# Optimization experiments

Measured on AMD Instinct MI355X. Metric: run time of the kernel, lower is better.

## Reference

```python
import jax, jax.numpy as jnp
import numpy as np

B, NV, NE = 32, 8192, 65536
SUBSTEPS = 8
DT = 0.01
K_SPRING = 1.0e4   # spring stiffness
CG_ITERS = 20      # fixed CG iterations for the implicit solve
EPS = 1e-12


def setup_inputs() -> dict:
    key = jax.random.key(0)
    k0, k1, k2, k3, k4, k5 = jax.random.split(key, 6)
    # small actuation signals per spring (rest-length modulation)
    input_action = jax.random.normal(k0, (B, NE), dtype=jnp.float32) * 0.05
    # random spring graph with guaranteed i != j
    edge_i = jax.random.randint(k1, (NE,), 0, NV, dtype=jnp.int32)
    off = jax.random.randint(k2, (NE,), 1, NV, dtype=jnp.int32)
    edge_j = ((edge_i + off) % NV).astype(jnp.int32)
    pos0 = jax.random.normal(k3, (B, NV, 3), dtype=jnp.float32) * 0.5
    vel0 = jnp.zeros((B, NV, 3), dtype=jnp.float32)
    # rest lengths near the initial configuration so the system starts close to equilibrium
    d0 = pos0[0, edge_i] - pos0[0, edge_j]
    rest_len = jnp.linalg.norm(d0, axis=-1) + 1e-2
    mass = jax.random.uniform(k4, (NV,), dtype=jnp.float32) + 0.5
    return {"input_action": input_action, "pos0": pos0, "vel0": vel0,
            "rest_len": rest_len, "mass": mass,
            "edge_i": edge_i, "edge_j": edge_j}


def _bdot(a, b):
    # per-batch inner product, keepdims for broadcasting: [B,1,1]
    return jnp.sum(a * b, axis=(1, 2), keepdims=True)


def _spring_force(pos, rest_eff, ei, ej):
    # pos: [B,NV,3], rest_eff: [B,NE]
    d = pos[:, ei] - pos[:, ej]                       # [B,NE,3]
    l = jnp.linalg.norm(d, axis=-1, keepdims=True)    # [B,NE,1]
    dirn = d / jnp.maximum(l, 1e-6)
    fe = -K_SPRING * (l - rest_eff[..., None]) * dirn # [B,NE,3]
    f = jnp.zeros_like(pos).at[:, ei].add(fe).at[:, ej].add(-fe)
    return f


def _matvec(x, mass, ei, ej):
    # A x = M x + dt^2 * k * L x  (graph Laplacian Hessian approximation)
    d = x[:, ei] - x[:, ej]
    Lx = jnp.zeros_like(x).at[:, ei].add(d).at[:, ej].add(-d)
    return mass[None, :, None] * x + (DT * DT * K_SPRING) * Lx


def _cg_solve(b, mass, ei, ej):
    x = jnp.zeros_like(b)
    r = b
    p = r
    rs = _bdot(r, r)

    def body(carry, _):
        x, r, p, rs = carry
        Ap = _matvec(p, mass, ei, ej)
        alpha = rs / (_bdot(p, Ap) + EPS)
        x = x + alpha * p
        r = r - alpha * Ap
        rs_new = _bdot(r, r)
        p = r + (rs_new / (rs + EPS)) * p
        return (x, r, p, rs_new), None

    (x, _, _, _), _ = jax.lax.scan(body, (x, r, p, rs), None, length=CG_ITERS)
    return x


def reference(input_action, pos0, vel0, rest_len, mass, edge_i, edge_j):
    gravity = jnp.array([0.0, -9.8, 0.0], dtype=pos0.dtype)
    rest_eff = rest_len[None, :] * (1.0 + input_action)  # actuated rest lengths [B,NE]
    m3 = mass[None, :, None]

    def step(carry, _):
        pos, vel = carry
        f = _spring_force(pos, rest_eff, edge_i, edge_j) + m3 * gravity
        b = m3 * vel + DT * f                  # implicit Euler RHS
        v_new = _cg_solve(b, mass, edge_i, edge_j)
        pos_new = pos + DT * v_new
        return (pos_new, v_new), pos_new

    _, traj = jax.lax.scan(step, (pos0, vel0), None, length=SUBSTEPS)
    # traj: [SUBSTEPS, B, NV, 3] -> [B, SUBSTEPS, NV, 3]
    return jnp.transpose(traj, (1, 0, 2, 3))
```

## Files before the change

kernel.cpp:

```cpp
#include <hip/hip_runtime.h>
#include <hip/hip_cooperative_groups.h>
#include <math.h>

namespace cg = cooperative_groups;

#define NVERT 8192
#define NEDGE 65536
#define NSUB 8
#define NCG 20
#define GRID 256
#define BLOCK 1024
#define DT 0.01f
#define KS 10000.0f
#define NGRP 16
#define GSIZE 16

struct Params {
  const float* action;
  const float* pos0;
  const float* vel0;
  const float* rest_len;
  const float* mass;
  const int* edge_i;
  const int* edge_j;
  float* out;
  float2* posXY;
  float*  posZ;
  float2 *QXY0, *QXY1;
  float  *QZ0,  *QZ1;
  float* rest_eff;
  int* adj_off;
  int* adjE_off;
  int* row_ptr;
  int* cursor;
  double* Pd;
  double* Gd;
  unsigned* bar;
};

union U64F2 { unsigned long long u; float2 f; };
union U32F  { unsigned u; float f; };
union U64D  { unsigned long long u; double d; };

__device__ __forceinline__ float2 ld2_dev(const float2* p) {
  U64F2 r;
  r.u = __hip_atomic_load((const unsigned long long*)p, __ATOMIC_RELAXED, __HIP_MEMORY_SCOPE_AGENT);
  return r.f;
}
__device__ __forceinline__ void st2_dev(float2* p, float2 v) {
  U64F2 r; r.f = v;
  __hip_atomic_store((unsigned long long*)p, r.u, __ATOMIC_RELAXED, __HIP_MEMORY_SCOPE_AGENT);
}
__device__ __forceinline__ float ldf_dev(const float* p) {
  U32F r;
  r.u = __hip_atomic_load((const unsigned*)p, __ATOMIC_RELAXED, __HIP_MEMORY_SCOPE_AGENT);
  return r.f;
}
__device__ __forceinline__ void stf_dev(float* p, float v) {
  U32F r; r.f = v;
  __hip_atomic_store((unsigned*)p, r.u, __ATOMIC_RELAXED, __HIP_MEMORY_SCOPE_AGENT);
}
__device__ __forceinline__ double lddbl_dev(const double* p) {
  U64D r;
  r.u = __hip_atomic_load((const unsigned long long*)p, __ATOMIC_RELAXED, __HIP_MEMORY_SCOPE_AGENT);
  return r.d;
}
__device__ __forceinline__ void stdbl_dev(double* p, double v) {
  U64D r; r.d = v;
  __hip_atomic_store((unsigned long long*)p, r.u, __ATOMIC_RELAXED, __HIP_MEMORY_SCOPE_AGENT);
}

__device__ __forceinline__ void fast_bar(unsigned* bar, unsigned ep) {
  __syncthreads();
  if (threadIdx.x == 0) {
    const unsigned g = blockIdx.x >> 4;
    __hip_atomic_fetch_add(bar + g * 32, 1u,
                           __ATOMIC_RELAXED, __HIP_MEMORY_SCOPE_AGENT);
    const unsigned tgt = GSIZE * ep;
    for (;;) {
      bool ok = true;
#pragma unroll
      for (int i = 0; i < NGRP; ++i)
        ok &= (__hip_atomic_load(bar + i * 32,
                                 __ATOMIC_RELAXED, __HIP_MEMORY_SCOPE_AGENT) >= tgt);
      if (ok) break;
      __builtin_amdgcn_s_sleep(1);
    }
  }
  __syncthreads();
}

__device__ __forceinline__ void fast_bar_red(unsigned* bar, unsigned ep,
                                             const double* Pd, double* Gd, int par,
                                             int* lflag) {
  __syncthreads();
  const unsigned g = blockIdx.x >> 4;
  if (threadIdx.x == 0) {
    const unsigned old = __hip_atomic_fetch_add(bar + g * 32, 1u,
                          __ATOMIC_RELAXED, __HIP_MEMORY_SCOPE_AGENT);
    *lflag = (old == GSIZE * ep - 1);
  }
  __syncthreads();
  if (*lflag) {
    if (threadIdx.x < 96) {
      const double* base = Pd + (size_t)par * 256 * 96 + (size_t)(g * GSIZE) * 96
                           + threadIdx.x;
      double s = 0.0;
#pragma unroll
      for (int j = 0; j < GSIZE; ++j) s += lddbl_dev(base + j * 96);
      stdbl_dev(&Gd[(size_t)par * NGRP * 96 + g * 96 + threadIdx.x], s);
    }
    __syncthreads();
    if (threadIdx.x == 0)
      __hip_atomic_store(bar + (NGRP + 1 + g) * 32, ep,
                         __ATOMIC_RELAXED, __HIP_MEMORY_SCOPE_AGENT);
  }
  if (threadIdx.x == 0) {
    for (;;) {
      bool ok = true;
#pragma unroll
      for (int i = 0; i < NGRP; ++i)
        ok &= (__hip_atomic_load(bar + (NGRP + 1 + i) * 32,
                                 __ATOMIC_RELAXED, __HIP_MEMORY_SCOPE_AGENT) >= ep);
      if (ok) break;
      __builtin_amdgcn_s_sleep(1);
    }
  }
  __syncthreads();
}

__device__ __forceinline__ void publish_store(double* Pd, int par, double d0, double d1,
                                              double d2, double* lds) {
  d0 += __shfl_down(d0, 32);
  d1 += __shfl_down(d1, 32);
  d2 += __shfl_down(d2, 32);
  const int lane = threadIdx.x & 63, w = threadIdx.x >> 6;
  if (lane < 32) {
    lds[w * 96 + lane] = d0;
    lds[w * 96 + 32 + lane] = d1;
    lds[w * 96 + 64 + lane] = d2;
  }
  __syncthreads();
  if (threadIdx.x < 96) {
    double s = 0.0;
#pragma unroll
    for (int ww = 0; ww < BLOCK / 64; ++ww) s += lds[ww * 96 + threadIdx.x];
    stdbl_dev(&Pd[(size_t)par * 256 * 96 + (size_t)blockIdx.x * 96 + threadIdx.x], s);
  }
}

__device__ __forceinline__ void reduce_small(const double* Gd, int par,
                                             double* lds_part, double* lds_acc) {
  const int tid = threadIdx.x;
  const double* base = Gd + (size_t)par * NGRP * 96;
  lds_part[tid] = lddbl_dev(base + tid);
  if (tid < NGRP * 96 - BLOCK)
    lds_part[BLOCK + tid] = lddbl_dev(base + BLOCK + tid);
  __syncthreads();
  if (tid < 96) {
    double s = 0.0;
#pragma unroll
    for (int g = 0; g < NGRP; ++g) s += lds_part[g * 96 + tid];
    lds_acc[tid] = s;
  }
  __syncthreads();
}

__global__ void __launch_bounds__(BLOCK) mass_spring_kernel(Params P) {
  cg::grid_group grid = cg::this_grid();
  __shared__ double lds_red[(BLOCK / 64) * 96];
  __shared__ double lds_part[NGRP * 96];
  __shared__ double lds_acc[96];
  __shared__ int lds_scan[BLOCK];
  __shared__ int lds_flag;

  const int tid = threadIdx.x;
  const int gtid = blockIdx.x * BLOCK + tid;
  const int b = tid & 31;
  const int v = gtid >> 5;
  const int vb = v * 32 + b;
  const int b8 = b * 8, b4 = b * 4;
  unsigned ep = 0;

  for (int i = gtid; i < NEDGE * 32; i += GRID * BLOCK) {
    const int e = i >> 5, bb = i & 31;
    P.rest_eff[e * 32 + bb] = P.rest_len[e] * (1.0f + P.action[bb * NEDGE + e]);
  }
  float3 pv, vv;
  pv.x = P.pos0[(b * NVERT + v) * 3 + 0];
  pv.y = P.pos0[(b * NVERT + v) * 3 + 1];
  pv.z = P.pos0[(b * NVERT + v) * 3 + 2];
  vv.x = P.vel0[(b * NVERT + v) * 3 + 0];
  vv.y = P.vel0[(b * NVERT + v) * 3 + 1];
  vv.z = P.vel0[(b * NVERT + v) * 3 + 2];
  st2_dev(&P.posXY[vb], make_float2(pv.x, pv.y));
  stf_dev(&P.posZ[vb], pv.z);
  if (gtid < NVERT) P.cursor[gtid] = 0;
  if (gtid < (2 * NGRP + 1) * 32) P.bar[gtid] = 0u;
  grid.sync();

  if (gtid < NEDGE) {
    atomicAdd(&P.cursor[P.edge_i[gtid]], 1);
    atomicAdd(&P.cursor[P.edge_j[gtid]], 1);
  }
  grid.sync();

  if (blockIdx.x == 0) {
    const int base = tid * (NVERT / BLOCK);
    int loc[NVERT / BLOCK];
    int sum = 0;
#pragma unroll
    for (int i = 0; i < NVERT / BLOCK; ++i) { loc[i] = P.cursor[base + i]; sum += loc[i]; }
    lds_scan[tid] = sum;
    __syncthreads();
    for (int off = 1; off < BLOCK; off <<= 1) {
      int t = 0;
      if (tid >= off) t = lds_scan[tid - off];
      __syncthreads();
      if (tid >= off) lds_scan[tid] += t;
      __syncthreads();
    }
    int run = lds_scan[tid] - sum;
#pragma unroll
    for (int i = 0; i < NVERT / BLOCK; ++i) {
      P.row_ptr[base + i] = run;
      P.cursor[base + i] = run;
      run += loc[i];
    }
    if (tid == BLOCK - 1) P.row_ptr[NVERT] = run;
  }
  grid.sync();

  if (gtid < NEDGE) {
    const int ei = P.edge_i[gtid], ej = P.edge_j[gtid];
    const int ai = atomicAdd(&P.cursor[ei], 1);
    P.adj_off[ai] = ej * 256; P.adjE_off[ai] = gtid * 128;
    const int aj = atomicAdd(&P.cursor[ej], 1);
    P.adj_off[aj] = ei * 256; P.adjE_off[aj] = gtid * 128;
  }
  grid.sync();

  const float m_v = P.mass[v];
  const int rbeg = P.row_ptr[v], rend = P.row_ptr[v + 1];
  const float degf = (float)(rend - rbeg);

  float2* qXYrd = P.QXY0; float2* qXYwr = P.QXY1;
  float*  qZrd  = P.QZ0;  float*  qZwr  = P.QZ1;
  int pub = 0;

  for (int s = 0; s < NSUB; ++s) {
    float fx = 0.f, fy = 0.f, fz = 0.f;
#pragma unroll 4
    for (int a = rbeg; a < rend; ++a) {
      const int off = P.adj_off[a];
      const float2 pxy = ld2_dev((const float2*)((const char*)P.posXY + off + b8));
      const float  puz = ldf_dev((const float*)((const char*)P.posZ + (off >> 1) + b4));
      const float re = *(const float*)((const char*)P.rest_eff + P.adjE_off[a] + b4);
      const float dx = pv.x - pxy.x, dy = pv.y - pxy.y, dz = pv.z - puz;
      const float l = sqrtf(dx * dx + dy * dy + dz * dz);
      const float coef = -KS * (l - re) / fmaxf(l, 1e-6f);
      fx += coef * dx; fy += coef * dy; fz += coef * dz;
    }
    float3 rv;
    rv.x = m_v * vv.x + DT * fx;
    rv.y = m_v * vv.y + DT * (fy - 9.8f * m_v);
    rv.z = m_v * vv.z + DT * fz;
    st2_dev(&qXYrd[vb], make_float2(rv.x, rv.y));
    stf_dev(&qZrd[vb], rv.z);
    float3 xacc = make_float3(0.f, 0.f, 0.f);
    float3 pc = rv;
    float3 ap;
    float3 Sr, Sp;
    fast_bar(P.bar, ++ep);

    for (int k = 0; k < NCG; ++k) {
      if (k == 0) {
        float sx = 0.f, sy = 0.f, sz = 0.f;
#pragma unroll 4
        for (int a = rbeg; a < rend; ++a) {
          const int off = P.adj_off[a];
          const float2 qxy = ld2_dev((const float2*)((const char*)qXYrd + off + b8));
          const float  qz  = ldf_dev((const float*)((const char*)qZrd + (off >> 1) + b4));
          sx += qxy.x; sy += qxy.y; sz += qz;
        }
        Sr = make_float3(sx, sy, sz);
        Sp = Sr;
        ap.x = (m_v + degf) * pc.x - Sp.x;
        ap.y = (m_v + degf) * pc.y - Sp.y;
        ap.z = (m_v + degf) * pc.z - Sp.z;
      } else {
        const double* gbase = P.Gd + (size_t)((pub + 1) & 1) * NGRP * 96;
        const double gval0 = lddbl_dev(gbase + tid);
        double gval1 = 0.0;
        if (tid < NGRP * 96 - BLOCK) gval1 = lddbl_dev(gbase + BLOCK + tid);
        float sx = 0.f, sy = 0.f, sz = 0.f;
#pragma unroll 4
        for (int a = rbeg; a < rend; ++a) {
          const int off = P.adj_off[a];
          const float2 qxy = ld2_dev((const float2*)((const char*)qXYrd + off + b8));
          const float  qz  = ldf_dev((const float*)((const char*)qZrd + (off >> 1) + b4));
          sx += qxy.x; sy += qxy.y; sz += qz;
        }
        lds_part[tid] = gval0;
        if (tid < NGRP * 96 - BLOCK) lds_part[BLOCK + tid] = gval1;
        __syncthreads();
        if (tid < 96) {
          double s = 0.0;
#pragma unroll
          for (int g = 0; g < NGRP; ++g) s += lds_part[g * 96 + tid];
          lds_acc[tid] = s;
        }
        __syncthreads();
        const double rsx = lds_acc[b];
        const double pq  = lds_acc[32 + b];
        const double qq  = lds_acc[64 + b];
        const float alpha = (float)(rsx / (pq + 1e-12));
        const double rs_rec = (double)alpha * (double)alpha * qq - rsx;
        const float beta = (float)(rs_rec / (rsx + 1e-12));
        xacc.x += alpha * pc.x; xacc.y += alpha * pc.y; xacc.z += alpha * pc.z;
        rv.x -= alpha * ap.x; rv.y -= alpha * ap.y; rv.z -= alpha * ap.z;
        Sr.x -= alpha * sx; Sr.y -= alpha * sy; Sr.z -= alpha * sz;
        pc.x = rv.x + beta * pc.x; pc.y = rv.y + beta * pc.y; pc.z = rv.z + beta * pc.z;
        Sp.x = Sr.x + beta * Sp.x; Sp.y = Sr.y + beta * Sp.y; Sp.z = Sr.z + beta * Sp.z;
        ap.x = (m_v + degf) * pc.x - Sp.x;
        ap.y = (m_v + degf) * pc.y - Sp.y;
        ap.z = (m_v + degf) * pc.z - Sp.z;
      }
      if (k != NCG - 1) {
        st2_dev(&qXYwr[vb], make_float2(ap.x, ap.y));
        stf_dev(&qZwr[vb], ap.z);
      }
      publish_store(P.Pd, pub & 1,
                    (double)(rv.x * rv.x) + (double)(rv.y * rv.y) + (double)(rv.z * rv.z),
                    (double)(pc.x * ap.x) + (double)(pc.y * ap.y) + (double)(pc.z * ap.z),
                    (double)(ap.x * ap.x) + (double)(ap.y * ap.y) + (double)(ap.z * ap.z),
                    lds_red);
      fast_bar_red(P.bar, ++ep, P.Pd, P.Gd, pub & 1, &lds_flag);
      ++pub;
      float2* t2 = qXYrd; qXYrd = qXYwr; qXYwr = t2;
      float*  t1 = qZrd;  qZrd  = qZwr;  qZwr  = t1;
    }

    {
      reduce_small(P.Gd, (pub + 1) & 1, lds_part, lds_acc);
      const double rsx = lds_acc[b];
      const double pq  = lds_acc[32 + b];
      const float alpha = (float)(rsx / (pq + 1e-12));
      xacc.x += alpha * pc.x; xacc.y += alpha * pc.y; xacc.z += alpha * pc.z;
      vv = xacc;
      pv.x += DT * vv.x; pv.y += DT * vv.y; pv.z += DT * vv.z;
      st2_dev(&P.posXY[vb], make_float2(pv.x, pv.y));
      stf_dev(&P.posZ[vb], pv.z);
      float* o = P.out + ((size_t)(b * NSUB + s) * NVERT + (size_t)v) * 3;
      o[0] = pv.x; o[1] = pv.y; o[2] = pv.z;
      fast_bar(P.bar, ++ep);
    }
  }
}

extern "C" void kernel_launch(void* const* d_in, const int* in_sizes, int n_in,
                              void* d_out, int out_size, void* d_ws, size_t ws_size,
                              hipStream_t stream) {
  Params P;
  P.action = (const float*)d_in[0];
  P.pos0 = (const float*)d_in[1];
  P.vel0 = (const float*)d_in[2];
  P.rest_len = (const float*)d_in[3];
  P.mass = (const float*)d_in[4];
  P.edge_i = (const int*)d_in[5];
  P.edge_j = (const int*)d_in[6];
  P.out = (float*)d_out;

  char* w = (char*)d_ws;
  auto alloc = [&](size_t bytes) {
    char* p = w;
    w += (bytes + 255) & ~(size_t)255;
    return p;
  };
  const size_t xy_bytes = (size_t)NVERT * 32 * sizeof(float2);
  const size_t z_bytes  = (size_t)NVERT * 32 * sizeof(float);
  P.posXY = (float2*)alloc(xy_bytes);
  P.posZ  = (float*)alloc(z_bytes);
  P.QXY0  = (float2*)alloc(xy_bytes);
  P.QXY1  = (float2*)alloc(xy_bytes);
  P.QZ0   = (float*)alloc(z_bytes);
  P.QZ1   = (float*)alloc(z_bytes);
  P.rest_eff = (float*)alloc((size_t)NEDGE * 32 * sizeof(float));
  P.adj_off  = (int*)alloc((size_t)2 * NEDGE * sizeof(int));
  P.adjE_off = (int*)alloc((size_t)2 * NEDGE * sizeof(int));
  P.row_ptr  = (int*)alloc((size_t)(NVERT + 1) * sizeof(int));
  P.cursor   = (int*)alloc((size_t)NVERT * sizeof(int));
  P.Pd       = (double*)alloc((size_t)2 * 256 * 96 * sizeof(double));
  P.Gd       = (double*)alloc((size_t)2 * NGRP * 96 * sizeof(double));
  P.bar      = (unsigned*)alloc((size_t)(2 * NGRP + 1) * 32 * sizeof(unsigned));

  void* args[] = { &P };
  hipLaunchCooperativeKernel(reinterpret_cast<void*>(mass_spring_kernel),
                             dim3(GRID), dim3(BLOCK), args, 0, stream);
}
```

Before: 2.089 ms.

## Replace two-level grid reduction with cumulative f64 atomics across striped rows

Each block now adds its per-batch CG dot-product partials with float64 atomics into one of four striped accumulator rows, instead of writing partials that group leaders combine hierarchically. The accumulators are never reset. Each block recovers the per-iteration value by subtracting the previous running total. This drops the second barrier phase and the group-level reduction pass, leaving a single plain grid barrier per CG iteration. In exchange it adds atomic contention on 384 doubles. Differencing running sums could also lose precision as the totals grow, and atomic ordering makes the reductions non-deterministic.

```diff
diff --git a/kernel.cpp b/kernel.cpp
--- a/kernel.cpp
+++ b/kernel.cpp
@@ -14,6 +14,7 @@
 #define KS 10000.0f
 #define NGRP 16
 #define GSIZE 16
+#define NROW 4
 
 struct Params {
   const float* action;
@@ -33,8 +34,7 @@
   int* adjE_off;
   int* row_ptr;
   int* cursor;
-  double* Pd;
-  double* Gd;
+  double* A;
   unsigned* bar;
 };
 
@@ -65,9 +65,9 @@
   r.u = __hip_atomic_load((const unsigned long long*)p, __ATOMIC_RELAXED, __HIP_MEMORY_SCOPE_AGENT);
   return r.d;
 }
-__device__ __forceinline__ void stdbl_dev(double* p, double v) {
-  U64D r; r.d = v;
-  __hip_atomic_store((unsigned long long*)p, r.u, __ATOMIC_RELAXED, __HIP_MEMORY_SCOPE_AGENT);
+
+__device__ __forceinline__ void atomic_add_f64_dev(double* p, double v) {
+  unsafeAtomicAdd(p, v);
 }
 
 __device__ __forceinline__ void fast_bar(unsigned* bar, unsigned ep) {
@@ -90,47 +90,8 @@
   __syncthreads();
 }
 
-__device__ __forceinline__ void fast_bar_red(unsigned* bar, unsigned ep,
-                                             const double* Pd, double* Gd, int par,
-                                             int* lflag) {
-  __syncthreads();
-  const unsigned g = blockIdx.x >> 4;
-  if (threadIdx.x == 0) {
-    const unsigned old = __hip_atomic_fetch_add(bar + g * 32, 1u,
-                          __ATOMIC_RELAXED, __HIP_MEMORY_SCOPE_AGENT);
-    *lflag = (old == GSIZE * ep - 1);
-  }
-  __syncthreads();
-  if (*lflag) {
-    if (threadIdx.x < 96) {
-      const double* base = Pd + (size_t)par * 256 * 96 + (size_t)(g * GSIZE) * 96
-                           + threadIdx.x;
-      double s = 0.0;
-#pragma unroll
-      for (int j = 0; j < GSIZE; ++j) s += lddbl_dev(base + j * 96);
-      stdbl_dev(&Gd[(size_t)par * NGRP * 96 + g * 96 + threadIdx.x], s);
-    }
-    __syncthreads();
-    if (threadIdx.x == 0)
-      __hip_atomic_store(bar + (NGRP + 1 + g) * 32, ep,
-                         __ATOMIC_RELAXED, __HIP_MEMORY_SCOPE_AGENT);
-  }
-  if (threadIdx.x == 0) {
-    for (;;) {
-      bool ok = true;
-#pragma unroll
-      for (int i = 0; i < NGRP; ++i)
-        ok &= (__hip_atomic_load(bar + (NGRP + 1 + i) * 32,
-                                 __ATOMIC_RELAXED, __HIP_MEMORY_SCOPE_AGENT) >= ep);
-      if (ok) break;
-      __builtin_amdgcn_s_sleep(1);
-    }
-  }
-  __syncthreads();
-}
-
-__device__ __forceinline__ void publish_store(double* Pd, int par, double d0, double d1,
-                                              double d2, double* lds) {
+__device__ __forceinline__ void publish_atomic(double* Arow, double d0, double d1,
+                                               double d2, double* lds) {
   d0 += __shfl_down(d0, 32);
   d1 += __shfl_down(d1, 32);
   d2 += __shfl_down(d2, 32);
@@ -145,34 +106,15 @@
     double s = 0.0;
 #pragma unroll
     for (int ww = 0; ww < BLOCK / 64; ++ww) s += lds[ww * 96 + threadIdx.x];
-    stdbl_dev(&Pd[(size_t)par * 256 * 96 + (size_t)blockIdx.x * 96 + threadIdx.x], s);
-  }
-}
-
-__device__ __forceinline__ void reduce_small(const double* Gd, int par,
-                                             double* lds_part, double* lds_acc) {
-  const int tid = threadIdx.x;
-  const double* base = Gd + (size_t)par * NGRP * 96;
-  lds_part[tid] = lddbl_dev(base + tid);
-  if (tid < NGRP * 96 - BLOCK)
-    lds_part[BLOCK + tid] = lddbl_dev(base + BLOCK + tid);
-  __syncthreads();
-  if (tid < 96) {
-    double s = 0.0;
-#pragma unroll
-    for (int g = 0; g < NGRP; ++g) s += lds_part[g * 96 + tid];
-    lds_acc[tid] = s;
-  }
-  __syncthreads();
+    atomic_add_f64_dev(Arow + threadIdx.x, s);
+  }
 }
 
 __global__ void __launch_bounds__(BLOCK) mass_spring_kernel(Params P) {
   cg::grid_group grid = cg::this_grid();
   __shared__ double lds_red[(BLOCK / 64) * 96];
-  __shared__ double lds_part[NGRP * 96];
   __shared__ double lds_acc[96];
   __shared__ int lds_scan[BLOCK];
-  __shared__ int lds_flag;
 
   const int tid = threadIdx.x;
   const int gtid = blockIdx.x * BLOCK + tid;
@@ -181,6 +123,8 @@
   const int vb = v * 32 + b;
   const int b8 = b * 8, b4 = b * 4;
   unsigned ep = 0;
+  double prevq = 0.0;
+  double* const Arow = P.A + (size_t)(blockIdx.x & (NROW - 1)) * 96;
 
   for (int i = gtid; i < NEDGE * 32; i += GRID * BLOCK) {
     const int e = i >> 5, bb = i & 31;
@@ -197,6 +141,7 @@
   stf_dev(&P.posZ[vb], pv.z);
   if (gtid < NVERT) P.cursor[gtid] = 0;
   if (gtid < (2 * NGRP + 1) * 32) P.bar[gtid] = 0u;
+  if (gtid < NROW * 96) P.A[gtid] = 0.0;
   grid.sync();
 
   if (gtid < NEDGE) {
@@ -246,7 +191,6 @@
 
   float2* qXYrd = P.QXY0; float2* qXYwr = P.QXY1;
   float*  qZrd  = P.QZ0;  float*  qZwr  = P.QZ1;
-  int pub = 0;
 
   for (int s = 0; s < NSUB; ++s) {
     float fx = 0.f, fy = 0.f, fz = 0.f;
@@ -289,10 +233,13 @@
         ap.y = (m_v + degf) * pc.y - Sp.y;
         ap.z = (m_v + degf) * pc.z - Sp.z;
       } else {
-        const double* gbase = P.Gd + (size_t)((pub + 1) & 1) * NGRP * 96;
-        const double gval0 = lddbl_dev(gbase + tid);
-        double gval1 = 0.0;
-        if (tid < NGRP * 96 - BLOCK) gval1 = lddbl_dev(gbase + BLOCK + tid);
+        double av0, av1, av2, av3;
+        if (tid < 96) {
+          av0 = lddbl_dev(P.A + tid);
+          av1 = lddbl_dev(P.A + 96 + tid);
+          av2 = lddbl_dev(P.A + 192 + tid);
+          av3 = lddbl_dev(P.A + 288 + tid);
+        }
         float sx = 0.f, sy = 0.f, sz = 0.f;
 #pragma unroll 4
         for (int a = rbeg; a < rend; ++a) {
@@ -301,14 +248,10 @@
           const float  qz  = ldf_dev((const float*)((const char*)qZrd + (off >> 1) + b4));
           sx += qxy.x; sy += qxy.y; sz += qz;
         }
-        lds_part[tid] = gval0;
-        if (tid < NGRP * 96 - BLOCK) lds_part[BLOCK + tid] = gval1;
-        __syncthreads();
         if (tid < 96) {
-          double s = 0.0;
-#pragma unroll
-          for (int g = 0; g < NGRP; ++g) s += lds_part[g * 96 + tid];
-          lds_acc[tid] = s;
+          const double anow = (av0 + av1) + (av2 + av3);
+          lds_acc[tid] = anow - prevq;
+          prevq = anow;
         }
         __syncthreads();
         const double rsx = lds_acc[b];
@@ -330,19 +273,24 @@
         st2_dev(&qXYwr[vb], make_float2(ap.x, ap.y));
         stf_dev(&qZwr[vb], ap.z);
       }
-      publish_store(P.Pd, pub & 1,
-                    (double)(rv.x * rv.x) + (double)(rv.y * rv.y) + (double)(rv.z * rv.z),
-                    (double)(pc.x * ap.x) + (double)(pc.y * ap.y) + (double)(pc.z * ap.z),
-                    (double)(ap.x * ap.x) + (double)(ap.y * ap.y) + (double)(ap.z * ap.z),
-                    lds_red);
-      fast_bar_red(P.bar, ++ep, P.Pd, P.Gd, pub & 1, &lds_flag);
-      ++pub;
+      publish_atomic(Arow,
+                     (double)(rv.x * rv.x) + (double)(rv.y * rv.y) + (double)(rv.z * rv.z),
+                     (double)(pc.x * ap.x) + (double)(pc.y * ap.y) + (double)(pc.z * ap.z),
+                     (double)(ap.x * ap.x) + (double)(ap.y * ap.y) + (double)(ap.z * ap.z),
+                     lds_red);
+      fast_bar(P.bar, ++ep);
       float2* t2 = qXYrd; qXYrd = qXYwr; qXYwr = t2;
       float*  t1 = qZrd;  qZrd  = qZwr;  qZwr  = t1;
     }
 
     {
-      reduce_small(P.Gd, (pub + 1) & 1, lds_part, lds_acc);
+      if (tid < 96) {
+        const double anow = (lddbl_dev(P.A + tid) + lddbl_dev(P.A + 96 + tid))
+                          + (lddbl_dev(P.A + 192 + tid) + lddbl_dev(P.A + 288 + tid));
+        lds_acc[tid] = anow - prevq;
+        prevq = anow;
+      }
+      __syncthreads();
       const double rsx = lds_acc[b];
       const double pq  = lds_acc[32 + b];
       const float alpha = (float)(rsx / (pq + 1e-12));
@@ -390,8 +338,7 @@
   P.adjE_off = (int*)alloc((size_t)2 * NEDGE * sizeof(int));
   P.row_ptr  = (int*)alloc((size_t)(NVERT + 1) * sizeof(int));
   P.cursor   = (int*)alloc((size_t)NVERT * sizeof(int));
-  P.Pd       = (double*)alloc((size_t)2 * 256 * 96 * sizeof(double));
-  P.Gd       = (double*)alloc((size_t)2 * NGRP * 96 * sizeof(double));
+  P.A        = (double*)alloc((size_t)NROW * 96 * sizeof(double));
   P.bar      = (unsigned*)alloc((size_t)(2 * NGRP + 1) * 32 * sizeof(unsigned));
 
   void* args[] = { &P };
```

Measured after the change: 2.208 ms. +5.7%, slower.
